# Kernel tuning notes

Measured on AMD Instinct MI355X. Metric: run time of the kernel, lower is better.

## Reference

```python
import jax, jax.numpy as jnp
import numpy as np

N = 100000      # nodes
E = 3200000     # edges
F_IN = 128      # num_features
H = 32          # hidden_dim (hard-coded in module)
C = 8           # num_classes
B = 128         # graphs in batch
BN_EPS = 1e-5


def setup_inputs() -> dict:
    key = jax.random.key(0)
    ks = jax.random.split(key, 24)
    s = 0.1
    inp = {
        "x": jax.random.normal(ks[0], (N, F_IN), jnp.float32),
        "edge_index": jax.random.randint(ks[1], (2, E), 0, N, dtype=jnp.int32),
        "batch": jnp.sort(jax.random.randint(ks[2], (N,), 0, B, dtype=jnp.int32)),
        # GINConv layer 0 (F_IN -> H -> H) MLP + BN params
        "w1_0": jax.random.normal(ks[3], (F_IN, H), jnp.float32) * s,
        "b1_0": jnp.zeros((H,), jnp.float32),
        "w2_0": jax.random.normal(ks[4], (H, H), jnp.float32) * s,
        "b2_0": jnp.zeros((H,), jnp.float32),
        "g_0": jnp.ones((H,), jnp.float32),
        "be_0": jnp.zeros((H,), jnp.float32),
        # GINConv layers 1..3 (H -> H -> H), stacked
        "w1s": jax.random.normal(ks[5], (3, H, H), jnp.float32) * s,
        "b1s": jnp.zeros((3, H), jnp.float32),
        "w2s": jax.random.normal(ks[6], (3, H, H), jnp.float32) * s,
        "b2s": jnp.zeros((3, H), jnp.float32),
        "gs": jnp.ones((3, H), jnp.float32),
        "bes": jnp.zeros((3, H), jnp.float32),
        # classifier head
        "fc1_w": jax.random.normal(ks[7], (H, H), jnp.float32) * s,
        "fc1_b": jnp.zeros((H,), jnp.float32),
        "fc2_w": jax.random.normal(ks[8], (H, C), jnp.float32) * s,
        "fc2_b": jnp.zeros((C,), jnp.float32),
    }
    return inp


def _gin_conv(h, src, dst, w1, b1, w2, b2):
    # GINConv with eps=0: MLP((1+eps)*x + sum_{j in N(i)} x_j)
    agg = jax.ops.segment_sum(h[src], dst, num_segments=N)  # scatter-add aggregation
    z = h + agg
    return jnp.maximum(z @ w1 + b1, 0.0) @ w2 + b2


def _batch_norm(h, gamma, beta):
    # BatchNorm1d in training mode: batch stats over node dim, biased variance
    mean = h.mean(axis=0)
    var = jnp.mean(jnp.square(h - mean), axis=0)
    return gamma * (h - mean) * jax.lax.rsqrt(var + BN_EPS) + beta


def reference(x, edge_index, batch, w1_0, b1_0, w2_0, b2_0, g_0, be_0,
              w1s, b1s, w2s, b2s, gs, bes, fc1_w, fc1_b, fc2_w, fc2_b):
    src, dst = edge_index[0], edge_index[1]
    h = _batch_norm(jnp.maximum(_gin_conv(x, src, dst, w1_0, b1_0, w2_0, b2_0), 0.0), g_0, be_0)
    for i in range(3):  # fixed small layer loop
        h = _batch_norm(jnp.maximum(_gin_conv(h, src, dst, w1s[i], b1s[i], w2s[i], b2s[i]), 0.0), gs[i], bes[i])
    # global_mean_pool over batch ids
    counts = jax.ops.segment_sum(jnp.ones((N,), h.dtype), batch, num_segments=B)
    pooled = jax.ops.segment_sum(h, batch, num_segments=B) / jnp.maximum(counts, 1.0)[:, None]
    h = jnp.maximum(pooled @ fc1_w + fc1_b, 0.0)
    # dropout p=0.5 treated as identity (eval-mode determinism)
    logits = h @ fc2_w + fc2_b
    return jax.nn.log_softmax(logits, axis=-1)
```

## Files before the change

kernel.cpp:

```cpp
#include <hip/hip_runtime.h>
#include <hip/hip_bf16.h>

#define NN   100000
#define EE   3200000
#define HH   32
#define BB   128
#define KMAX 96
#define NB   1024
#define SPAN 98
#define EBLK 256
#define CHUNK 12500

static constexpr size_t PAIRS_OFF  = 0;
static constexpr size_t Q_OFF      = 0;
static constexpr size_t AGG_OFF    = 6400000;
static constexpr size_t H_OFF      = 19200000;
static constexpr size_t HIST_OFF   = 26000000;
static constexpr size_t START_OFF  = 27100000;
static constexpr size_t BBASE_OFF  = 28200000;
static constexpr size_t TOT_OFF    = 28210000;
static constexpr size_t CSR_OFF    = 38400000;
static constexpr size_t CNT_OFF    = 76800000;
static constexpr size_t STATS_OFF  = 77200000;
static constexpr size_t BNAB_OFF   = 77200256;
static constexpr size_t POOLED_OFF = 77200512;
static constexpr size_t PCNT_OFF   = 77216896;
static constexpr size_t ZERO_OFF   = POOLED_OFF;
static constexpr size_t ZERO_BYTES = 16896;

__global__ __launch_bounds__(256) void hist_kernel(const int* __restrict__ ei,
                                                   int* __restrict__ hist) {
    __shared__ int lh[NB];
    int tid = threadIdx.x, blk = blockIdx.x;
    for (int i = tid; i < NB; i += 256) lh[i] = 0;
    __syncthreads();
    int e0 = blk * CHUNK;
    for (int e = e0 + tid; e < e0 + CHUNK; e += 256) {
        int d = ei[EE + e];
        atomicAdd(&lh[d / SPAN], 1);
    }
    __syncthreads();
    for (int i = tid; i < NB; i += 256) hist[blk * NB + i] = lh[i];
}

__global__ __launch_bounds__(64) void totals_kernel(const int* __restrict__ hist,
                                                    int* __restrict__ tot) {
    int b = blockIdx.x * 64 + threadIdx.x;
    int s = 0;
    for (int blk = 0; blk < EBLK; blk++) s += hist[blk * NB + b];
    tot[b] = s;
}

__global__ __launch_bounds__(1024) void scan_kernel(const int* __restrict__ tot,
                                                    int* __restrict__ bbase) {
    __shared__ int sm[NB];
    int t = threadIdx.x;
    int mine = tot[t];
    sm[t] = mine;
    __syncthreads();
    for (int off = 1; off < NB; off <<= 1) {
        int v = (t >= off) ? sm[t - off] : 0;
        __syncthreads();
        sm[t] += v;
        __syncthreads();
    }
    bbase[t] = sm[t] - mine;
    if (t == NB - 1) bbase[NB] = sm[t];
}

__global__ __launch_bounds__(128) void starts_kernel(const int* __restrict__ hist,
                                                     const int* __restrict__ bbase,
                                                     int* __restrict__ start) {
    int b = blockIdx.x * 128 + threadIdx.x;
    int run = bbase[b];
    for (int blk = 0; blk < EBLK; blk++) {
        start[blk * NB + b] = run;
        run += hist[blk * NB + b];
    }
}

__global__ __launch_bounds__(256) void scatter_kernel(const int* __restrict__ ei,
                                                      const int* __restrict__ start,
                                                      int2* __restrict__ pairs) {
    __shared__ int loff[NB];
    int tid = threadIdx.x, blk = blockIdx.x;
    for (int i = tid; i < NB; i += 256) loff[i] = start[blk * NB + i];
    __syncthreads();
    int e0 = blk * CHUNK;
    for (int e = e0 + tid; e < e0 + CHUNK; e += 256) {
        int s = ei[e];
        int d = ei[EE + e];
        int slot = atomicAdd(&loff[d / SPAN], 1);
        pairs[slot] = make_int2(s, d);
    }
}

__global__ __launch_bounds__(256) void csr_from_bins_kernel(const int2* __restrict__ pairs,
                                                            const int* __restrict__ bbase,
                                                            int* __restrict__ cnt,
                                                            int* __restrict__ csr) {
    __shared__ int lcnt[SPAN];
    __shared__ int lcsr[SPAN * KMAX];
    int b = blockIdx.x;
    int tid = threadIdx.x;
    for (int i = tid; i < SPAN; i += 256) lcnt[i] = 0;
    __syncthreads();
    int p0 = bbase[b], p1 = bbase[b + 1];
    int base = b * SPAN;
    for (int i = p0 + tid; i < p1; i += 256) {
        int2 p = pairs[i];
        int ld = p.y - base;
        int slot = atomicAdd(&lcnt[ld], 1);
        if (slot < KMAX) lcsr[ld * KMAX + slot] = p.x;
    }
    __syncthreads();
    for (int i = tid; i < SPAN; i += 256) {
        int n = base + i;
        if (n < NN) cnt[n] = lcnt[i];
    }
    int span_here = min(SPAN, NN - base);
    if (span_here <= 0) return;
    int maxw = span_here * KMAX;
    int* gout = csr + (size_t)base * KMAX;
    for (int i = tid; i < maxw; i += 256) gout[i] = lcsr[i];
}

__device__ __forceinline__ unsigned bf16rn(float f) {
    unsigned b = __float_as_uint(f);
    return (b + 0x7fffu + ((b >> 16) & 1u)) >> 16;
}

template <int FIN>
__global__ __launch_bounds__(256) void proj_kernel(const float* __restrict__ hin,
                                                   const float* __restrict__ w1,
                                                   const float* __restrict__ b1,
                                                   const float* __restrict__ bnab,
                                                   unsigned* __restrict__ qb,
                                                   float* __restrict__ agg,
                                                   float* __restrict__ stats) {
    int tid = threadIdx.x;
    if (blockIdx.x == 0 && tid < 64) stats[tid] = 0.f;
    int n = blockIdx.x * 256 + tid;
    if (n >= NN) return;
    float acc[32];
#pragma unroll
    for (int c = 0; c < 32; c++) acc[c] = 0.f;
    const float4* h4 = (const float4*)(hin + (size_t)n * FIN);
    for (int jj = 0; jj < FIN; jj += 32) {
        float hv[32];
#pragma unroll
        for (int k = 0; k < 8; k++) {
            float4 v = h4[jj / 4 + k];
            hv[4 * k] = v.x; hv[4 * k + 1] = v.y; hv[4 * k + 2] = v.z; hv[4 * k + 3] = v.w;
        }
        if constexpr (FIN == 32) {
#pragma unroll
            for (int j = 0; j < 32; j++) hv[j] = fmaf(hv[j], bnab[j], bnab[32 + j]);
        }
#pragma unroll 4
        for (int j = 0; j < 32; j++) {
            float hvj = hv[j];
            const float* wrow = w1 + (size_t)(jj + j) * 32;
#pragma unroll
            for (int c = 0; c < 32; c++) acc[c] = fmaf(hvj, wrow[c], acc[c]);
        }
    }
    uint4* qr = (uint4*)(qb + (size_t)n * 16);
#pragma unroll
    for (int k = 0; k < 4; k++) {
        uint4 u;
        u.x = bf16rn(acc[8*k+0]) | (bf16rn(acc[8*k+1]) << 16);
        u.y = bf16rn(acc[8*k+2]) | (bf16rn(acc[8*k+3]) << 16);
        u.z = bf16rn(acc[8*k+4]) | (bf16rn(acc[8*k+5]) << 16);
        u.w = bf16rn(acc[8*k+6]) | (bf16rn(acc[8*k+7]) << 16);
        qr[k] = u;
    }
    float4* ar = (float4*)(agg + (size_t)n * 32);
#pragma unroll
    for (int k = 0; k < 8; k++) {
        float4 av;
        av.x = acc[4*k]   + b1[4*k];
        av.y = acc[4*k+1] + b1[4*k+1];
        av.z = acc[4*k+2] + b1[4*k+2];
        av.w = acc[4*k+3] + b1[4*k+3];
        ar[k] = av;
    }
}

__global__ __launch_bounds__(256) void gather_kernel(const uint4* __restrict__ q4,
                                                     const int* __restrict__ csr,
                                                     const int* __restrict__ cnt,
                                                     float4* __restrict__ agg4) {
    int t = blockIdx.x * 256 + threadIdx.x;
    int n = t >> 2;
    if (n >= NN) return;
    int p = t & 3;
    int d = min(cnt[n], KMAX);
    const int* lst = csr + (size_t)n * KMAX;
    float a[8];
#pragma unroll
    for (int k = 0; k < 8; k++) a[k] = 0.f;
    int i = 0;
    for (; i + 4 <= d; i += 4) {
        int s0 = lst[i], s1 = lst[i+1], s2 = lst[i+2], s3 = lst[i+3];
        uint4 v0 = q4[(size_t)s0 * 4 + p];
        uint4 v1 = q4[(size_t)s1 * 4 + p];
        uint4 v2 = q4[(size_t)s2 * 4 + p];
        uint4 v3 = q4[(size_t)s3 * 4 + p];
#pragma unroll
        for (int w = 0; w < 4; w++) {
            unsigned ux = (w==0)?v0.x:(w==1)?v1.x:(w==2)?v2.x:v3.x;
            unsigned uy = (w==0)?v0.y:(w==1)?v1.y:(w==2)?v2.y:v3.y;
            unsigned uz = (w==0)?v0.z:(w==1)?v1.z:(w==2)?v2.z:v3.z;
            unsigned uw = (w==0)?v0.w:(w==1)?v1.w:(w==2)?v2.w:v3.w;
            a[0] += __uint_as_float(ux << 16);
            a[1] += __uint_as_float(ux & 0xffff0000u);
            a[2] += __uint_as_float(uy << 16);
            a[3] += __uint_as_float(uy & 0xffff0000u);
            a[4] += __uint_as_float(uz << 16);
            a[5] += __uint_as_float(uz & 0xffff0000u);
            a[6] += __uint_as_float(uw << 16);
            a[7] += __uint_as_float(uw & 0xffff0000u);
        }
    }
    for (; i < d; i++) {
        uint4 v = q4[(size_t)lst[i] * 4 + p];
        a[0] += __uint_as_float(v.x << 16);
        a[1] += __uint_as_float(v.x & 0xffff0000u);
        a[2] += __uint_as_float(v.y << 16);
        a[3] += __uint_as_float(v.y & 0xffff0000u);
        a[4] += __uint_as_float(v.z << 16);
        a[5] += __uint_as_float(v.z & 0xffff0000u);
        a[6] += __uint_as_float(v.w << 16);
        a[7] += __uint_as_float(v.w & 0xffff0000u);
    }
    size_t o = (size_t)n * 8 + p * 2;
    float4 g0 = agg4[o], g1 = agg4[o + 1];
    g0.x += a[0]; g0.y += a[1]; g0.z += a[2]; g0.w += a[3];
    g1.x += a[4]; g1.y += a[5]; g1.z += a[6]; g1.w += a[7];
    agg4[o] = g0; agg4[o + 1] = g1;
}

__global__ __launch_bounds__(256) void mlp_kernel(const float* __restrict__ agg,
                                                  const float* __restrict__ w2,
                                                  const float* __restrict__ b2,
                                                  float* __restrict__ r,
                                                  float* __restrict__ stats) {
    __shared__ float tile[256 * 33];
    __shared__ float ps[8 * 32];
    __shared__ float pq[8 * 32];
    int tid = threadIdx.x;
    int n = blockIdx.x * 256 + tid;
    float rc[32];
    if (n < NN) {
        float u[32];
        const float4* a4 = (const float4*)(agg + (size_t)n * 32);
#pragma unroll
        for (int k = 0; k < 8; k++) {
            float4 v = a4[k];
            u[4*k]   = fmaxf(v.x, 0.f);
            u[4*k+1] = fmaxf(v.y, 0.f);
            u[4*k+2] = fmaxf(v.z, 0.f);
            u[4*k+3] = fmaxf(v.w, 0.f);
        }
#pragma unroll
        for (int c = 0; c < 32; c++) rc[c] = b2[c];
#pragma unroll 4
        for (int j = 0; j < 32; j++) {
            float uj = u[j];
            const float* wrow = w2 + (size_t)j * 32;
#pragma unroll
            for (int c = 0; c < 32; c++) rc[c] = fmaf(uj, wrow[c], rc[c]);
        }
#pragma unroll
        for (int c = 0; c < 32; c++) rc[c] = fmaxf(rc[c], 0.f);
        float4* rr = (float4*)(r + (size_t)n * 32);
#pragma unroll
        for (int k = 0; k < 8; k++) {
            float4 v; v.x = rc[4*k]; v.y = rc[4*k+1]; v.z = rc[4*k+2]; v.w = rc[4*k+3];
            rr[k] = v;
        }
    } else {
#pragma unroll
        for (int c = 0; c < 32; c++) rc[c] = 0.f;
    }
#pragma unroll
    for (int c = 0; c < 32; c++) tile[tid * 33 + c] = rc[c];
    __syncthreads();
    {
        int c = tid & 31, rb = tid >> 5;
        float s = 0.f, sq = 0.f;
        for (int it = 0; it < 32; it++) {
            float v = tile[(rb * 32 + it) * 33 + c];
            s += v; sq += v * v;
        }
        ps[rb * 32 + c] = s; pq[rb * 32 + c] = sq;
    }
    __syncthreads();
    if (tid < 32) {
        float s = 0.f, sq = 0.f;
#pragma unroll
        for (int rb = 0; rb < 8; rb++) { s += ps[rb * 32 + tid]; sq += pq[rb * 32 + tid]; }
        atomicAdd(&stats[tid], s);
        atomicAdd(&stats[32 + tid], sq);
    }
}

__global__ void bnfin_kernel(const float* __restrict__ stats, const float* __restrict__ g,
                             const float* __restrict__ be, float* __restrict__ bnab) {
    int c = threadIdx.x;
    if (c >= 32) return;
    float mean = stats[c] * (1.0f / NN);
    float var  = fmaxf(stats[32 + c] * (1.0f / NN) - mean * mean, 0.f);
    float a = g[c] * rsqrtf(var + 1e-5f);
    bnab[c] = a;
    bnab[32 + c] = be[c] - mean * a;
}

#define PR 128
__global__ __launch_bounds__(256) void pool_kernel(const float* __restrict__ h,
                                                   const int* __restrict__ batch,
                                                   float* __restrict__ pooled,
                                                   float* __restrict__ pcnt) {
    int t = blockIdx.x * 256 + threadIdx.x;
    int c = t & 31;
    int g = t >> 5;
    int r0 = g * PR;
    if (r0 >= NN) return;
    int r1 = min(r0 + PR, NN);
    int cur = batch[r0];
    float acc = 0.f, cn = 0.f;
    for (int rr = r0; rr < r1; rr++) {
        int b = batch[rr];
        if (b != cur) {
            atomicAdd(&pooled[cur * 32 + c], acc);
            if (c == 0) atomicAdd(&pcnt[cur], cn);
            acc = 0.f; cn = 0.f; cur = b;
        }
        acc += h[(size_t)rr * 32 + c];
        cn += 1.f;
    }
    atomicAdd(&pooled[cur * 32 + c], acc);
    if (c == 0) atomicAdd(&pcnt[cur], cn);
}

__global__ __launch_bounds__(128) void head_kernel(const float* __restrict__ pooled,
                                                   const float* __restrict__ pcnt,
                                                   const float* __restrict__ bnab,
                                                   const float* __restrict__ fc1w,
                                                   const float* __restrict__ fc1b,
                                                   const float* __restrict__ fc2w,
                                                   const float* __restrict__ fc2b,
                                                   float* __restrict__ out) {
    int g = threadIdx.x;
    if (g >= BB) return;
    float inv = 1.f / fmaxf(pcnt[g], 1.f);
    float xv[32];
#pragma unroll
    for (int c = 0; c < 32; c++) xv[c] = fmaf(bnab[c], pooled[g * 32 + c] * inv, bnab[32 + c]);
    float u[32];
#pragma unroll 4
    for (int k = 0; k < 32; k++) {
        float s = fc1b[k];
#pragma unroll
        for (int c = 0; c < 32; c++) s = fmaf(xv[c], fc1w[c * 32 + k], s);
        u[k] = fmaxf(s, 0.f);
    }
    float l[8];
#pragma unroll
    for (int o = 0; o < 8; o++) {
        float s = fc2b[o];
#pragma unroll
        for (int k = 0; k < 32; k++) s = fmaf(u[k], fc2w[k * 8 + o], s);
        l[o] = s;
    }
    float m = l[0];
#pragma unroll
    for (int o = 1; o < 8; o++) m = fmaxf(m, l[o]);
    float se = 0.f;
#pragma unroll
    for (int o = 0; o < 8; o++) se += expf(l[o] - m);
    float lse = logf(se) + m;
#pragma unroll
    for (int o = 0; o < 8; o++) out[g * 8 + o] = l[o] - lse;
}

extern "C" void kernel_launch(void* const* d_in, const int* in_sizes, int n_in,
                              void* d_out, int out_size, void* d_ws, size_t ws_size,
                              hipStream_t stream) {
    const float* x    = (const float*)d_in[0];
    const int*   ei   = (const int*)d_in[1];
    const int*   batch= (const int*)d_in[2];
    const float* w1_0 = (const float*)d_in[3];
    const float* b1_0 = (const float*)d_in[4];
    const float* w2_0 = (const float*)d_in[5];
    const float* b2_0 = (const float*)d_in[6];
    const float* g_0  = (const float*)d_in[7];
    const float* be_0 = (const float*)d_in[8];
    const float* w1s  = (const float*)d_in[9];
    const float* b1s  = (const float*)d_in[10];
    const float* w2s  = (const float*)d_in[11];
    const float* b2s  = (const float*)d_in[12];
    const float* gs   = (const float*)d_in[13];
    const float* bes  = (const float*)d_in[14];
    const float* fc1w = (const float*)d_in[15];
    const float* fc1b = (const float*)d_in[16];
    const float* fc2w = (const float*)d_in[17];
    const float* fc2b = (const float*)d_in[18];
    float* out = (float*)d_out;

    char* ws = (char*)d_ws;
    int2*     pairs = (int2*)(ws + PAIRS_OFF);
    unsigned* qb    = (unsigned*)(ws + Q_OFF);
    float*    agg   = (float*)(ws + AGG_OFF);
    float*    h     = (float*)(ws + H_OFF);
    int*      hist  = (int*)(ws + HIST_OFF);
    int*      start = (int*)(ws + START_OFF);
    int*      bbase = (int*)(ws + BBASE_OFF);
    int*      tot   = (int*)(ws + TOT_OFF);
    int*      csr   = (int*)(ws + CSR_OFF);
    int*      cnt   = (int*)(ws + CNT_OFF);
    float*    stats = (float*)(ws + STATS_OFF);
    float*    bnab  = (float*)(ws + BNAB_OFF);
    float*    pooled= (float*)(ws + POOLED_OFF);
    float*    pcnt  = (float*)(ws + PCNT_OFF);

    hipMemsetAsync(ws + ZERO_OFF, 0, ZERO_BYTES, stream);

    hist_kernel<<<EBLK, 256, 0, stream>>>(ei, hist);
    totals_kernel<<<NB / 64, 64, 0, stream>>>(hist, tot);
    scan_kernel<<<1, NB, 0, stream>>>(tot, bbase);
    starts_kernel<<<NB / 128, 128, 0, stream>>>(hist, bbase, start);
    scatter_kernel<<<EBLK, 256, 0, stream>>>(ei, start, pairs);
    csr_from_bins_kernel<<<NB, 256, 0, stream>>>(pairs, bbase, cnt, csr);

    const int nblk = (NN + 255) / 256;
    const int gblk = (NN * 4 + 255) / 256;

    proj_kernel<128><<<nblk, 256, 0, stream>>>(x, w1_0, b1_0, nullptr, qb, agg, stats);
    gather_kernel<<<gblk, 256, 0, stream>>>((const uint4*)qb, csr, cnt, (float4*)agg);
    mlp_kernel<<<nblk, 256, 0, stream>>>(agg, w2_0, b2_0, h, stats);
    bnfin_kernel<<<1, 64, 0, stream>>>(stats, g_0, be_0, bnab);

    for (int i = 0; i < 3; i++) {
        proj_kernel<32><<<nblk, 256, 0, stream>>>(h, w1s + i * 1024, b1s + i * 32, bnab, qb, agg, stats);
        gather_kernel<<<gblk, 256, 0, stream>>>((const uint4*)qb, csr, cnt, (float4*)agg);
        mlp_kernel<<<nblk, 256, 0, stream>>>(agg, w2s + i * 1024, b2s + i * 32, h, stats);
        bnfin_kernel<<<1, 64, 0, stream>>>(stats, gs + i * 32, bes + i * 32, bnab);
    }

    int pthreads = ((NN + PR - 1) / PR) * 32;
    pool_kernel<<<(pthreads + 255) / 256, 256, 0, stream>>>(h, batch, pooled, pcnt);
    head_kernel<<<1, 128, 0, stream>>>(pooled, pcnt, bnab, fc1w, fc1b, fc2w, fc2b, out);
}
```

Before: 648.2 us.

## Fuse gather with second MLP and compact CSR to variable-length offsets

Replaces the padded per-node CSR (KMAX slots per node) with a compact offset/source layout, built by packing src and local dst into one int during binning. The neighbour gather, self term, bias, ReLU, second matmul and BN statistics now run in a single kernel that stages z in shared memory. This removes the fp32 agg buffer round trip and the separate mlp pass. The self term now comes from the bf16-quantised projection instead of fp32, and a serial prefix in thread 0 plus a binary search per output slot add some build cost.

```diff
diff --git a/kernel.cpp b/kernel.cpp
--- a/kernel.cpp
+++ b/kernel.cpp
@@ -10,21 +10,21 @@
 #define SPAN 98
 #define EBLK 256
 #define CHUNK 12500
-
-static constexpr size_t PAIRS_OFF  = 0;
+#define GN   64
+
 static constexpr size_t Q_OFF      = 0;
-static constexpr size_t AGG_OFF    = 6400000;
-static constexpr size_t H_OFF      = 19200000;
-static constexpr size_t HIST_OFF   = 26000000;
-static constexpr size_t START_OFF  = 27100000;
-static constexpr size_t BBASE_OFF  = 28200000;
-static constexpr size_t TOT_OFF    = 28210000;
-static constexpr size_t CSR_OFF    = 38400000;
-static constexpr size_t CNT_OFF    = 76800000;
-static constexpr size_t STATS_OFF  = 77200000;
-static constexpr size_t BNAB_OFF   = 77200256;
-static constexpr size_t POOLED_OFF = 77200512;
-static constexpr size_t PCNT_OFF   = 77216896;
+static constexpr size_t H_OFF      = 6400000;
+static constexpr size_t EPACK_OFF  = 19200000;
+static constexpr size_t SRC_OFF    = 32000000;
+static constexpr size_t OFF_OFF    = 44800000;
+static constexpr size_t HIST_OFF   = 45300000;
+static constexpr size_t START_OFF  = 46400000;
+static constexpr size_t BBASE_OFF  = 47500000;
+static constexpr size_t TOT_OFF    = 47600000;
+static constexpr size_t STATS_OFF  = 47700000;
+static constexpr size_t BNAB_OFF   = 47700256;
+static constexpr size_t POOLED_OFF = 47700512;
+static constexpr size_t PCNT_OFF   = 47716896;
 static constexpr size_t ZERO_OFF   = POOLED_OFF;
 static constexpr size_t ZERO_BYTES = 16896;
 
@@ -81,7 +81,7 @@
 
 __global__ __launch_bounds__(256) void scatter_kernel(const int* __restrict__ ei,
                                                       const int* __restrict__ start,
-                                                      int2* __restrict__ pairs) {
+                                                      int* __restrict__ epack) {
     __shared__ int loff[NB];
     int tid = threadIdx.x, blk = blockIdx.x;
     for (int i = tid; i < NB; i += 256) loff[i] = start[blk * NB + i];
@@ -90,39 +90,56 @@
     for (int e = e0 + tid; e < e0 + CHUNK; e += 256) {
         int s = ei[e];
         int d = ei[EE + e];
-        int slot = atomicAdd(&loff[d / SPAN], 1);
-        pairs[slot] = make_int2(s, d);
-    }
-}
-
-__global__ __launch_bounds__(256) void csr_from_bins_kernel(const int2* __restrict__ pairs,
-                                                            const int* __restrict__ bbase,
-                                                            int* __restrict__ cnt,
-                                                            int* __restrict__ csr) {
+        int b = d / SPAN;
+        int slot = atomicAdd(&loff[b], 1);
+        epack[slot] = s | ((d - b * SPAN) << 20);
+    }
+}
+
+__global__ __launch_bounds__(256) void csr_compact_kernel(const int* __restrict__ epack,
+                                                          const int* __restrict__ bbase,
+                                                          int* __restrict__ off,
+                                                          int* __restrict__ srcs) {
     __shared__ int lcnt[SPAN];
+    __shared__ int lbase[SPAN + 1];
     __shared__ int lcsr[SPAN * KMAX];
     int b = blockIdx.x;
     int tid = threadIdx.x;
+    int base = b * SPAN;
+    int span_here = NN - base;
+    if (span_here <= 0) return;
+    if (span_here > SPAN) span_here = SPAN;
     for (int i = tid; i < SPAN; i += 256) lcnt[i] = 0;
     __syncthreads();
     int p0 = bbase[b], p1 = bbase[b + 1];
-    int base = b * SPAN;
     for (int i = p0 + tid; i < p1; i += 256) {
-        int2 p = pairs[i];
-        int ld = p.y - base;
+        int w = epack[i];
+        int ld = w >> 20;
         int slot = atomicAdd(&lcnt[ld], 1);
-        if (slot < KMAX) lcsr[ld * KMAX + slot] = p.x;
-    }
-    __syncthreads();
-    for (int i = tid; i < SPAN; i += 256) {
-        int n = base + i;
-        if (n < NN) cnt[n] = lcnt[i];
-    }
-    int span_here = min(SPAN, NN - base);
-    if (span_here <= 0) return;
-    int maxw = span_here * KMAX;
-    int* gout = csr + (size_t)base * KMAX;
-    for (int i = tid; i < maxw; i += 256) gout[i] = lcsr[i];
+        if (slot < KMAX) lcsr[ld * KMAX + slot] = w & 0xFFFFF;
+    }
+    __syncthreads();
+    if (tid == 0) {
+        int run = 0;
+        for (int i = 0; i < span_here; i++) {
+            lbase[i] = run;
+            int c = lcnt[i]; if (c > KMAX) c = KMAX;
+            run += c;
+        }
+        lbase[span_here] = run;
+    }
+    __syncthreads();
+    for (int i = tid; i < span_here; i += 256) off[base + i] = p0 + lbase[i];
+    if (base <= NN && NN < base + SPAN && tid == 0) off[NN] = p0 + lbase[span_here];
+    int m = lbase[span_here];
+    for (int j = tid; j < m; j += 256) {
+        int lo = 0, hi = span_here - 1;
+        while (lo < hi) {
+            int mid = (lo + hi + 1) >> 1;
+            if (lbase[mid] <= j) lo = mid; else hi = mid - 1;
+        }
+        srcs[p0 + j] = lcsr[lo * KMAX + (j - lbase[lo])];
+    }
 }
 
 __device__ __forceinline__ unsigned bf16rn(float f) {
@@ -133,10 +150,8 @@
 template <int FIN>
 __global__ __launch_bounds__(256) void proj_kernel(const float* __restrict__ hin,
                                                    const float* __restrict__ w1,
-                                                   const float* __restrict__ b1,
                                                    const float* __restrict__ bnab,
                                                    unsigned* __restrict__ qb,
-                                                   float* __restrict__ agg,
                                                    float* __restrict__ stats) {
     int tid = threadIdx.x;
     if (blockIdx.x == 0 && tid < 64) stats[tid] = 0.f;
@@ -175,134 +190,106 @@
         u.w = bf16rn(acc[8*k+6]) | (bf16rn(acc[8*k+7]) << 16);
         qr[k] = u;
     }
-    float4* ar = (float4*)(agg + (size_t)n * 32);
-#pragma unroll
-    for (int k = 0; k < 8; k++) {
-        float4 av;
-        av.x = acc[4*k]   + b1[4*k];
-        av.y = acc[4*k+1] + b1[4*k+1];
-        av.z = acc[4*k+2] + b1[4*k+2];
-        av.w = acc[4*k+3] + b1[4*k+3];
-        ar[k] = av;
-    }
-}
-
-__global__ __launch_bounds__(256) void gather_kernel(const uint4* __restrict__ q4,
-                                                     const int* __restrict__ csr,
-                                                     const int* __restrict__ cnt,
-                                                     float4* __restrict__ agg4) {
-    int t = blockIdx.x * 256 + threadIdx.x;
-    int n = t >> 2;
-    if (n >= NN) return;
-    int p = t & 3;
-    int d = min(cnt[n], KMAX);
-    const int* lst = csr + (size_t)n * KMAX;
-    float a[8];
-#pragma unroll
-    for (int k = 0; k < 8; k++) a[k] = 0.f;
-    int i = 0;
-    for (; i + 4 <= d; i += 4) {
-        int s0 = lst[i], s1 = lst[i+1], s2 = lst[i+2], s3 = lst[i+3];
-        uint4 v0 = q4[(size_t)s0 * 4 + p];
-        uint4 v1 = q4[(size_t)s1 * 4 + p];
-        uint4 v2 = q4[(size_t)s2 * 4 + p];
-        uint4 v3 = q4[(size_t)s3 * 4 + p];
-#pragma unroll
-        for (int w = 0; w < 4; w++) {
-            unsigned ux = (w==0)?v0.x:(w==1)?v1.x:(w==2)?v2.x:v3.x;
-            unsigned uy = (w==0)?v0.y:(w==1)?v1.y:(w==2)?v2.y:v3.y;
-            unsigned uz = (w==0)?v0.z:(w==1)?v1.z:(w==2)?v2.z:v3.z;
-            unsigned uw = (w==0)?v0.w:(w==1)?v1.w:(w==2)?v2.w:v3.w;
-            a[0] += __uint_as_float(ux << 16);
-            a[1] += __uint_as_float(ux & 0xffff0000u);
-            a[2] += __uint_as_float(uy << 16);
-            a[3] += __uint_as_float(uy & 0xffff0000u);
-            a[4] += __uint_as_float(uz << 16);
-            a[5] += __uint_as_float(uz & 0xffff0000u);
-            a[6] += __uint_as_float(uw << 16);
-            a[7] += __uint_as_float(uw & 0xffff0000u);
-        }
-    }
-    for (; i < d; i++) {
-        uint4 v = q4[(size_t)lst[i] * 4 + p];
-        a[0] += __uint_as_float(v.x << 16);
-        a[1] += __uint_as_float(v.x & 0xffff0000u);
-        a[2] += __uint_as_float(v.y << 16);
-        a[3] += __uint_as_float(v.y & 0xffff0000u);
-        a[4] += __uint_as_float(v.z << 16);
-        a[5] += __uint_as_float(v.z & 0xffff0000u);
-        a[6] += __uint_as_float(v.w << 16);
-        a[7] += __uint_as_float(v.w & 0xffff0000u);
-    }
-    size_t o = (size_t)n * 8 + p * 2;
-    float4 g0 = agg4[o], g1 = agg4[o + 1];
-    g0.x += a[0]; g0.y += a[1]; g0.z += a[2]; g0.w += a[3];
-    g1.x += a[4]; g1.y += a[5]; g1.z += a[6]; g1.w += a[7];
-    agg4[o] = g0; agg4[o + 1] = g1;
-}
-
-__global__ __launch_bounds__(256) void mlp_kernel(const float* __restrict__ agg,
-                                                  const float* __restrict__ w2,
-                                                  const float* __restrict__ b2,
-                                                  float* __restrict__ r,
-                                                  float* __restrict__ stats) {
-    __shared__ float tile[256 * 33];
+}
+
+__global__ __launch_bounds__(256) void gmlp_kernel(const uint4* __restrict__ q4,
+                                                   const int* __restrict__ srcs,
+                                                   const int* __restrict__ off,
+                                                   const float* __restrict__ b1,
+                                                   const float* __restrict__ w2,
+                                                   const float* __restrict__ b2,
+                                                   float* __restrict__ hout,
+                                                   float* __restrict__ stats) {
+    __shared__ float zs[GN * 33];
+    __shared__ float lw2[32 * 32];
     __shared__ float ps[8 * 32];
     __shared__ float pq[8 * 32];
     int tid = threadIdx.x;
-    int n = blockIdx.x * 256 + tid;
-    float rc[32];
+    for (int i = tid; i < 1024; i += 256) lw2[i] = w2[i];
+    int g = tid >> 2, p = tid & 3;
+    int n = blockIdx.x * GN + g;
+    float a[8];
+#pragma unroll
+    for (int k = 0; k < 8; k++) a[k] = 0.f;
     if (n < NN) {
-        float u[32];
-        const float4* a4 = (const float4*)(agg + (size_t)n * 32);
-#pragma unroll
-        for (int k = 0; k < 8; k++) {
-            float4 v = a4[k];
-            u[4*k]   = fmaxf(v.x, 0.f);
-            u[4*k+1] = fmaxf(v.y, 0.f);
-            u[4*k+2] = fmaxf(v.z, 0.f);
-            u[4*k+3] = fmaxf(v.w, 0.f);
-        }
-#pragma unroll
-        for (int c = 0; c < 32; c++) rc[c] = b2[c];
-#pragma unroll 4
+        int o0 = off[n], o1 = off[n + 1];
+        const int* lst = srcs + o0;
+        int d = o1 - o0;
+        int i = 0;
+        for (; i + 4 <= d; i += 4) {
+            int s0 = lst[i], s1 = lst[i+1], s2 = lst[i+2], s3 = lst[i+3];
+            uint4 v0 = q4[(size_t)s0 * 4 + p];
+            uint4 v1 = q4[(size_t)s1 * 4 + p];
+            uint4 v2 = q4[(size_t)s2 * 4 + p];
+            uint4 v3 = q4[(size_t)s3 * 4 + p];
+#pragma unroll
+            for (int w = 0; w < 4; w++) {
+                unsigned ux = (w==0)?v0.x:(w==1)?v1.x:(w==2)?v2.x:v3.x;
+                unsigned uy = (w==0)?v0.y:(w==1)?v1.y:(w==2)?v2.y:v3.y;
+                unsigned uz = (w==0)?v0.z:(w==1)?v1.z:(w==2)?v2.z:v3.z;
+                unsigned uw = (w==0)?v0.w:(w==1)?v1.w:(w==2)?v2.w:v3.w;
+                a[0] += __uint_as_float(ux << 16);
+                a[1] += __uint_as_float(ux & 0xffff0000u);
+                a[2] += __uint_as_float(uy << 16);
+                a[3] += __uint_as_float(uy & 0xffff0000u);
+                a[4] += __uint_as_float(uz << 16);
+                a[5] += __uint_as_float(uz & 0xffff0000u);
+                a[6] += __uint_as_float(uw << 16);
+                a[7] += __uint_as_float(uw & 0xffff0000u);
+            }
+        }
+        for (; i < d; i++) {
+            uint4 v = q4[(size_t)lst[i] * 4 + p];
+            a[0] += __uint_as_float(v.x << 16);
+            a[1] += __uint_as_float(v.x & 0xffff0000u);
+            a[2] += __uint_as_float(v.y << 16);
+            a[3] += __uint_as_float(v.y & 0xffff0000u);
+            a[4] += __uint_as_float(v.z << 16);
+            a[5] += __uint_as_float(v.z & 0xffff0000u);
+            a[6] += __uint_as_float(v.w << 16);
+            a[7] += __uint_as_float(v.w & 0xffff0000u);
+        }
+        {
+            uint4 v = q4[(size_t)n * 4 + p];
+            a[0] += __uint_as_float(v.x << 16);
+            a[1] += __uint_as_float(v.x & 0xffff0000u);
+            a[2] += __uint_as_float(v.y << 16);
+            a[3] += __uint_as_float(v.y & 0xffff0000u);
+            a[4] += __uint_as_float(v.z << 16);
+            a[5] += __uint_as_float(v.z & 0xffff0000u);
+            a[6] += __uint_as_float(v.w << 16);
+            a[7] += __uint_as_float(v.w & 0xffff0000u);
+#pragma unroll
+            for (int k = 0; k < 8; k++) a[k] += b1[p * 8 + k];
+        }
+    }
+#pragma unroll
+    for (int k = 0; k < 8; k++) zs[g * 33 + p * 8 + k] = a[k];
+    __syncthreads();
+    int c = tid & 31, rg = tid >> 5;
+    float s = 0.f, sq = 0.f;
+    for (int r = rg; r < GN; r += 8) {
+        int n2 = blockIdx.x * GN + r;
+        float v = b2[c];
+#pragma unroll
         for (int j = 0; j < 32; j++) {
-            float uj = u[j];
-            const float* wrow = w2 + (size_t)j * 32;
-#pragma unroll
-            for (int c = 0; c < 32; c++) rc[c] = fmaf(uj, wrow[c], rc[c]);
-        }
-#pragma unroll
-        for (int c = 0; c < 32; c++) rc[c] = fmaxf(rc[c], 0.f);
-        float4* rr = (float4*)(r + (size_t)n * 32);
-#pragma unroll
-        for (int k = 0; k < 8; k++) {
-            float4 v; v.x = rc[4*k]; v.y = rc[4*k+1]; v.z = rc[4*k+2]; v.w = rc[4*k+3];
-            rr[k] = v;
-        }
-    } else {
-#pragma unroll
-        for (int c = 0; c < 32; c++) rc[c] = 0.f;
-    }
-#pragma unroll
-    for (int c = 0; c < 32; c++) tile[tid * 33 + c] = rc[c];
-    __syncthreads();
-    {
-        int c = tid & 31, rb = tid >> 5;
-        float s = 0.f, sq = 0.f;
-        for (int it = 0; it < 32; it++) {
-            float v = tile[(rb * 32 + it) * 33 + c];
+            float u = fmaxf(zs[r * 33 + j], 0.f);
+            v = fmaf(u, lw2[j * 32 + c], v);
+        }
+        v = fmaxf(v, 0.f);
+        if (n2 < NN) {
+            hout[(size_t)n2 * 32 + c] = v;
             s += v; sq += v * v;
         }
-        ps[rb * 32 + c] = s; pq[rb * 32 + c] = sq;
-    }
+    }
+    ps[rg * 32 + c] = s; pq[rg * 32 + c] = sq;
     __syncthreads();
     if (tid < 32) {
-        float s = 0.f, sq = 0.f;
-#pragma unroll
-        for (int rb = 0; rb < 8; rb++) { s += ps[rb * 32 + tid]; sq += pq[rb * 32 + tid]; }
-        atomicAdd(&stats[tid], s);
-        atomicAdd(&stats[32 + tid], sq);
+        float ts = 0.f, tq = 0.f;
+#pragma unroll
+        for (int rb = 0; rb < 8; rb++) { ts += ps[rb * 32 + tid]; tq += pq[rb * 32 + tid]; }
+        atomicAdd(&stats[tid], ts);
+        atomicAdd(&stats[32 + tid], tq);
     }
 }
 
@@ -410,16 +397,15 @@
     float* out = (float*)d_out;
 
     char* ws = (char*)d_ws;
-    int2*     pairs = (int2*)(ws + PAIRS_OFF);
     unsigned* qb    = (unsigned*)(ws + Q_OFF);
-    float*    agg   = (float*)(ws + AGG_OFF);
     float*    h     = (float*)(ws + H_OFF);
+    int*      epack = (int*)(ws + EPACK_OFF);
+    int*      srcs  = (int*)(ws + SRC_OFF);
+    int*      off   = (int*)(ws + OFF_OFF);
     int*      hist  = (int*)(ws + HIST_OFF);
     int*      start = (int*)(ws + START_OFF);
     int*      bbase = (int*)(ws + BBASE_OFF);
     int*      tot   = (int*)(ws + TOT_OFF);
-    int*      csr   = (int*)(ws + CSR_OFF);
-    int*      cnt   = (int*)(ws + CNT_OFF);
     float*    stats = (float*)(ws + STATS_OFF);
     float*    bnab  = (float*)(ws + BNAB_OFF);
     float*    pooled= (float*)(ws + POOLED_OFF);
@@ -431,21 +417,20 @@
     totals_kernel<<<NB / 64, 64, 0, stream>>>(hist, tot);
     scan_kernel<<<1, NB, 0, stream>>>(tot, bbase);
     starts_kernel<<<NB / 128, 128, 0, stream>>>(hist, bbase, start);
-    scatter_kernel<<<EBLK, 256, 0, stream>>>(ei, start, pairs);
-    csr_from_bins_kernel<<<NB, 256, 0, stream>>>(pairs, bbase, cnt, csr);
+    scatter_kernel<<<EBLK, 256, 0, stream>>>(ei, start, epack);
+    csr_compact_kernel<<<NB, 256, 0, stream>>>(epack, bbase, off, srcs);
 
     const int nblk = (NN + 255) / 256;
-    const int gblk = (NN * 4 + 255) / 256;
-
-    proj_kernel<128><<<nblk, 256, 0, stream>>>(x, w1_0, b1_0, nullptr, qb, agg, stats);
-    gather_kernel<<<gblk, 256, 0, stream>>>((const uint4*)qb, csr, cnt, (float4*)agg);
-    mlp_kernel<<<nblk, 256, 0, stream>>>(agg, w2_0, b2_0, h, stats);
+    const int gblk = (NN + GN - 1) / GN;
+
+    proj_kernel<128><<<nblk, 256, 0, stream>>>(x, w1_0, nullptr, qb, stats);
+    gmlp_kernel<<<gblk, 256, 0, stream>>>((const uint4*)qb, srcs, off, b1_0, w2_0, b2_0, h, stats);
     bnfin_kernel<<<1, 64, 0, stream>>>(stats, g_0, be_0, bnab);
 
     for (int i = 0; i < 3; i++) {
-        proj_kernel<32><<<nblk, 256, 0, stream>>>(h, w1s + i * 1024, b1s + i * 32, bnab, qb, agg, stats);
-        gather_kernel<<<gblk, 256, 0, stream>>>((const uint4*)qb, csr, cnt, (float4*)agg);
-        mlp_kernel<<<nblk, 256, 0, stream>>>(agg, w2s + i * 1024, b2s + i * 32, h, stats);
+        proj_kernel<32><<<nblk, 256, 0, stream>>>(h, w1s + i * 1024, bnab, qb, stats);
+        gmlp_kernel<<<gblk, 256, 0, stream>>>((const uint4*)qb, srcs, off, b1s + i * 32,
+                                              w2s + i * 1024, b2s + i * 32, h, stats);
         bnfin_kernel<<<1, 64, 0, stream>>>(stats, gs + i * 32, bes + i * 32, bnab);
     }
 
```

Result: slower. 765.8 us (+18.1%).
